# Kernel tuning notes

Measured on AMD Instinct MI355X. Metric: run time of the kernel, lower is better.

The kernel has to match this reference:

```python
import jax, jax.numpy as jnp
import numpy as np

B, T, L, D, H = 4, 1024, 1024, 1024, 16
HS = D // H          # head_size = 64
ROT = HS // 2        # rotary_ndims = 32


def setup_inputs() -> dict:
    key = jax.random.key(0)
    ks = jax.random.split(key, 8)
    x = jax.random.normal(ks[0], (B, T, D), dtype=jnp.float32)
    memory = jax.random.normal(ks[1], (B, L, D), dtype=jnp.float32)
    # RotaryEmbedding(rotary_ndims): inv_freq over ROT/2 freqs, emb = cat(freqs, freqs)
    inv_freq = 1.0 / (10000.0 ** (np.arange(0, ROT, 2, dtype=np.float32) / ROT))
    t = np.arange(T, dtype=np.float32)
    freqs = np.einsum('i,j->ij', t, inv_freq)            # [T, ROT/2]
    emb = np.concatenate([freqs, freqs], axis=-1)        # [T, ROT]
    RoPE = jnp.asarray(np.stack([np.cos(emb), np.sin(emb)]), dtype=jnp.float32)  # [2, T, ROT]
    s = 0.02
    Wq = jax.random.normal(ks[2], (D, D), dtype=jnp.float32) * s
    Wk = jax.random.normal(ks[3], (D, D), dtype=jnp.float32) * s
    Wv = jax.random.normal(ks[4], (D, D), dtype=jnp.float32) * s
    Wo = jax.random.normal(ks[5], (D, D), dtype=jnp.float32) * s
    bq = jnp.zeros((D,), jnp.float32)
    bk = jnp.zeros((D,), jnp.float32)
    bv = jnp.zeros((D,), jnp.float32)
    bo = jnp.zeros((D,), jnp.float32)
    return {"x": x, "memory": memory, "RoPE": RoPE,
            "Wq": Wq, "bq": bq, "Wk": Wk, "bk": bk,
            "Wv": Wv, "bv": bv, "Wo": Wo, "bo": bo}


def _rotate_half(u):
    u1, u2 = u[..., : u.shape[-1] // 2], u[..., u.shape[-1] // 2:]
    return jnp.concatenate([-u2, u1], axis=-1)


def _heads(y, n):  # [B, N, D] -> [B, H, N, HS]
    b = y.shape[0]
    return y.reshape(b, n, H, HS).transpose(0, 2, 1, 3)


def _attn(q, k, v):
    scale = 1.0 / jnp.sqrt(jnp.asarray(k.shape[-1], q.dtype))
    att = jnp.einsum('bhtd,bhsd->bhts', q, k) * scale
    att = jax.nn.softmax(att, axis=-1)
    return jnp.einsum('bhts,bhsd->bhtd', att, v)


def reference(x, memory, RoPE, Wq, bq, Wk, bk, Wv, bv, Wo, bo):
    b, t, d = x.shape
    l = memory.shape[1]
    cos, sin = RoPE[0][:t], RoPE[1][:t]  # [T, ROT], broadcasts over [B,H,T,ROT]

    # ---- self-attention with partial rotary ----
    q = _heads(x @ Wq.T + bq, t)
    k = _heads(x @ Wk.T + bk, t)
    v = _heads(x @ Wv.T + bv, t)
    q_rot, q_pass = q[..., :ROT], q[..., ROT:]
    k_rot, k_pass = k[..., :ROT], k[..., ROT:]
    q_rot = q_rot * cos + _rotate_half(q_rot) * sin
    k_rot = k_rot * cos + _rotate_half(k_rot) * sin
    q = jnp.concatenate([q_rot, q_pass], axis=-1)
    k = jnp.concatenate([k_rot, k_pass], axis=-1)
    y = _attn(q, k, v)                                   # [B,H,T,HS]
    y = y.transpose(0, 2, 1, 3).reshape(b, t, d)

    # ---- cross-attention (no rotary) ----
    q = _heads(y @ Wq.T + bq, t)
    k = _heads(memory @ Wk.T + bk, l)
    v = _heads(memory @ Wv.T + bv, l)
    y = _attn(q, k, v)
    y = y.transpose(0, 2, 1, 3).reshape(b, t, d)
    return y @ Wo.T + bo
```

## Files before the change

### kernel.cpp

```cpp
#include <hip/hip_runtime.h>

typedef unsigned short u16;
typedef __attribute__((ext_vector_type(8))) unsigned short ushort8;
typedef __attribute__((ext_vector_type(4))) unsigned short ushort4v;
typedef __attribute__((ext_vector_type(4))) float f32x4;
typedef __bf16 bf16x8 __attribute__((ext_vector_type(8)));


__device__ __forceinline__ u16 f2bf(float f) {
    unsigned u = __builtin_bit_cast(unsigned, f);
    unsigned r = u + 0x7fffu + ((u >> 16) & 1u);
    return (u16)(r >> 16);
}
__device__ __forceinline__ float bf2f(u16 h) {
    unsigned u = ((unsigned)h) << 16;
    return __builtin_bit_cast(float, u);
}

typedef const __attribute__((address_space(1))) unsigned gu32;
typedef __attribute__((address_space(3))) unsigned lu32;
__device__ __forceinline__ void gload16(const void* g, void* l) {
    __builtin_amdgcn_global_load_lds((gu32*)g, (lu32*)l, 16, 0, 0);
}

__global__ void k_f2b(const float4* __restrict__ in, u16* __restrict__ out, int n4) {
    int i = blockIdx.x * blockDim.x + threadIdx.x;
    if (i >= n4) return;
    float4 v = in[i];
    ushort4v r = { f2bf(v.x), f2bf(v.y), f2bf(v.z), f2bf(v.w) };
    *(ushort4v*)(out + (size_t)i * 4) = r;
}

template<int NSEG, int OUTBF>
__global__ __launch_bounds__(256) void k_gemm(const u16* __restrict__ Ap,
        const u16* __restrict__ w0, const u16* __restrict__ w1, const u16* __restrict__ w2,
        const float* __restrict__ b0, const float* __restrict__ b1, const float* __restrict__ b2,
        void* __restrict__ Cp, int colbase, int ldc) {
    __shared__ ushort8 sA[2][512];
    __shared__ ushort8 sB[2][512];
    const int tid = threadIdx.x, lane = tid & 63, w = tid >> 6;
    const int wr = w >> 1, wc = w & 1;

    const int nbx = gridDim.x;
    const int orig = blockIdx.y * nbx + blockIdx.x;
    const int qq = (nbx * gridDim.y) >> 3;
    const int logical = (orig & 7) * qq + (orig >> 3);
    const int bx = logical % nbx;
    const int m0 = (logical / nbx) * 128;

    const u16* W = w0; const float* bias = b0;
    if (NSEG >= 2 && bx >= 8)  { W = w1; bias = b1; }
    if (NSEG >= 3 && bx >= 16) { W = w2; bias = b2; }
    const int n0w = (bx & 7) * 128;
    const int outc0 = colbase + bx * 128;

    f32x4 acc[4][4] = {};

    const u16* asrc = Ap + (size_t)(m0 + 32 * w + (lane & 15)) * 1024 + (lane >> 4) * 8;
    const u16* bsrc = W  + (size_t)(n0w + 32 * w + (lane & 15)) * 1024 + (lane >> 4) * 8;

#define G_STAGE(p, kt) do { \
    gload16(asrc + (kt),             &sA[p][w * 128]); \
    gload16(asrc + (kt) + 16 * 1024, &sA[p][w * 128 + 64]); \
    gload16(bsrc + (kt),             &sB[p][w * 128]); \
    gload16(bsrc + (kt) + 16 * 1024, &sB[p][w * 128 + 64]); } while (0)

#define G_COMPUTE(p) do { \
    __builtin_amdgcn_s_barrier(); \
    asm volatile("" ::: "memory"); \
    bf16x8 af[4], bfr[4]; \
    for (int i = 0; i < 4; i++) af[i]  = __builtin_bit_cast(bf16x8, sA[p][(wr * 4 + i) * 64 + lane]); \
    for (int j = 0; j < 4; j++) bfr[j] = __builtin_bit_cast(bf16x8, sB[p][(wc * 4 + j) * 64 + lane]); \
    for (int i = 0; i < 4; i++) \
        for (int j = 0; j < 4; j++) \
            acc[i][j] = __builtin_amdgcn_mfma_f32_16x16x32_bf16(af[i], bfr[j], acc[i][j], 0, 0, 0); \
    asm volatile("" ::: "memory"); \
    __builtin_amdgcn_s_barrier(); } while (0)

    G_STAGE(0, 0);
    for (int t = 0; t < 30; t += 2) {
        G_STAGE(1, (t + 1) * 32);
        asm volatile("s_waitcnt vmcnt(4)" ::: "memory");
        G_COMPUTE(0);
        G_STAGE(0, (t + 2) * 32);
        asm volatile("s_waitcnt vmcnt(4)" ::: "memory");
        G_COMPUTE(1);
    }
    G_STAGE(1, 31 * 32);
    asm volatile("s_waitcnt vmcnt(4)" ::: "memory");
    G_COMPUTE(0);
    asm volatile("s_waitcnt vmcnt(0)" ::: "memory");
    G_COMPUTE(1);
#undef G_STAGE
#undef G_COMPUTE

    const int er = (lane >> 4) * 4, ec = lane & 15;
    for (int i = 0; i < 4; i++) {
        int grow_base = m0 + wr * 64 + i * 16 + er;
        for (int j = 0; j < 4; j++) {
            int cl = wc * 64 + j * 16 + ec;
            float bia = bias[n0w + cl];
            int gcol = outc0 + cl;
            for (int e = 0; e < 4; e++) {
                float v = acc[i][j][e] + bia;
                if (OUTBF) ((u16*)Cp)[(size_t)(grow_base + e) * ldc + gcol] = f2bf(v);
                else       ((float*)Cp)[(size_t)(grow_base + e) * ldc + gcol] = v;
            }
        }
    }
}

__global__ void k_rope(u16* __restrict__ QKV, const float* __restrict__ rope) {
    int idx = blockIdx.x * blockDim.x + threadIdx.x;
    int p = idx & 15;
    int h = (idx >> 4) & 15;
    int row = idx >> 8;
    int t = row & 1023;
    float c1 = rope[t * 32 + p];
    float c2 = rope[t * 32 + p + 16];
    const float* sinp = rope + 32768;
    float s1 = sinp[t * 32 + p];
    float s2 = sinp[t * 32 + p + 16];
    size_t base = (size_t)row * 3072 + h * 64;
    float u1 = bf2f(QKV[base + p]), u2 = bf2f(QKV[base + p + 16]);
    QKV[base + p]      = f2bf(u1 * c1 - u2 * s1);
    QKV[base + p + 16] = f2bf(u2 * c2 + u1 * s2);
    size_t kb = base + 1024;
    u1 = bf2f(QKV[kb + p]); u2 = bf2f(QKV[kb + p + 16]);
    QKV[kb + p]      = f2bf(u1 * c1 - u2 * s1);
    QKV[kb + p + 16] = f2bf(u2 * c2 + u1 * s2);
}

__global__ __launch_bounds__(256) void k_vt(const u16* __restrict__ Vb, u16* __restrict__ VTo) {
    __shared__ u16 tile[64][72];
    const int tid = threadIdx.x, lane = tid & 63, w = tid >> 6;
    const int sx = blockIdx.x, bh = blockIdx.y;
    const int b = bh >> 4, h = bh & 15;
    const u16* Vp = Vb + (size_t)(b * 1024 + sx * 64) * 3072 + h * 64;
    for (int it = 0; it < 2; it++) {
        int c = tid + it * 256, r = c >> 3, dc = c & 7;
        *(ushort8*)&tile[r][dc * 8] = *(const ushort8*)(Vp + (size_t)r * 3072 + dc * 8);
    }
    __syncthreads();
    u16* outp = VTo + (size_t)(bh * 64 + lane) * 1024 + sx * 64;
    for (int it = 0; it < 2; it++) {
        int sc = w + it * 4;
        ushort8 tv;
        for (int e = 0; e < 8; e++) tv[e] = tile[sc * 8 + e][lane];
        *(ushort8*)(outp + sc * 8) = tv;
    }
}

__global__ __launch_bounds__(256) void k_attn(const u16* __restrict__ Q, const u16* __restrict__ K,
                                              const u16* __restrict__ VTb, u16* __restrict__ O) {
    __shared__ ushort8 sK[2][512];
    __shared__ ushort8 sV[2][512];
    __shared__ ushort8 sP[512];

    const int tid = threadIdx.x, lane = tid & 63, w = tid >> 6;
    const int qt = blockIdx.x, h = blockIdx.y, b = blockIdx.z;
    const u16* Qh = Q + (size_t)(b * 1024 + qt * 64) * 3072 + h * 64;
    const u16* Kh = K + (size_t)(b * 1024) * 3072 + h * 64;
    const u16* VTh = VTb + (size_t)((b * 16 + h) * 64) * 1024;

    const u16* qa = Qh + (size_t)(16 * w + (lane & 15)) * 3072 + (lane >> 4) * 8;
    bf16x8 qf0 = __builtin_bit_cast(bf16x8, *(const ushort8*)qa);
    bf16x8 qf1 = __builtin_bit_cast(bf16x8, *(const ushort8*)(qa + 32));

    float m[4] = { -1e30f, -1e30f, -1e30f, -1e30f };
    float lsum[4] = { 0.f, 0.f, 0.f, 0.f };
    f32x4 o[4] = {};
    const float LS = 0.18033688011112042f;

    const int mrow = (lane >> 4) * 4;
    const int hi8 = (lane & 15) >> 3;
    const int se7 = lane & 7;

    const u16* ks = Kh + (size_t)(16 * w + (lane & 15)) * 3072 + (lane >> 4) * 8;
    const u16* vs = VTh + (size_t)(16 * w + (lane & 15)) * 1024 + (lane >> 4) * 8;

#define A_STAGE(p, s0) do { \
    gload16(ks + (size_t)(s0) * 3072,        &sK[p][w * 128]); \
    gload16(ks + (size_t)((s0) + 32) * 3072, &sK[p][w * 128 + 64]); \
    gload16(vs + (s0),                       &sV[p][w * 128]); \
    gload16(vs + (s0) + 32,                  &sV[p][w * 128 + 64]); } while (0)

#define A_COMPUTE(p) do { \
    __builtin_amdgcn_s_barrier(); \
    asm volatile("" ::: "memory"); \
    f32x4 sfr[4]; \
    for (int cb = 0; cb < 4; cb++) { \
        bf16x8 k0 = __builtin_bit_cast(bf16x8, sK[p][cb * 128 + lane]); \
        bf16x8 k1 = __builtin_bit_cast(bf16x8, sK[p][cb * 128 + 64 + lane]); \
        f32x4 a = {}; \
        a = __builtin_amdgcn_mfma_f32_16x16x32_bf16(qf0, k0, a, 0, 0, 0); \
        a = __builtin_amdgcn_mfma_f32_16x16x32_bf16(qf1, k1, a, 0, 0, 0); \
        sfr[cb] = a; \
    } \
    float rescale[4]; \
    for (int e = 0; e < 4; e++) { \
        float mx = fmaxf(fmaxf(sfr[0][e], sfr[1][e]), fmaxf(sfr[2][e], sfr[3][e])); \
        for (int off = 1; off < 16; off <<= 1) mx = fmaxf(mx, __shfl_xor(mx, off, 64)); \
        float mn = fmaxf(m[e], mx); \
        float r = __builtin_amdgcn_exp2f((m[e] - mn) * LS); \
        float rowsum = 0.f; \
        for (int cb = 0; cb < 4; cb++) { \
            float pv = __builtin_amdgcn_exp2f((sfr[cb][e] - mn) * LS); \
            sfr[cb][e] = pv; \
            rowsum += pv; \
        } \
        for (int off = 1; off < 16; off <<= 1) rowsum += __shfl_xor(rowsum, off, 64); \
        lsum[e] = lsum[e] * r + rowsum; \
        m[e] = mn; \
        rescale[e] = r; \
    } \
    for (int db = 0; db < 4; db++) \
        for (int e = 0; e < 4; e++) o[db][e] *= rescale[e]; \
    u16* sPw = ((u16*)sP) + w * 1024; \
    for (int cb = 0; cb < 4; cb++) { \
        int schunk = cb * 2 + hi8; \
        int cbase = (schunk >> 2) * 64 + (schunk & 3) * 16; \
        for (int e = 0; e < 4; e++) \
            sPw[(cbase + mrow + e) * 8 + se7] = f2bf(sfr[cb][e]); \
    } \
    bf16x8 pf0 = __builtin_bit_cast(bf16x8, sP[w * 128 + lane]); \
    bf16x8 pf1 = __builtin_bit_cast(bf16x8, sP[w * 128 + 64 + lane]); \
    for (int db = 0; db < 4; db++) { \
        bf16x8 v0 = __builtin_bit_cast(bf16x8, sV[p][db * 128 + lane]); \
        bf16x8 v1 = __builtin_bit_cast(bf16x8, sV[p][db * 128 + 64 + lane]); \
        o[db] = __builtin_amdgcn_mfma_f32_16x16x32_bf16(pf0, v0, o[db], 0, 0, 0); \
        o[db] = __builtin_amdgcn_mfma_f32_16x16x32_bf16(pf1, v1, o[db], 0, 0, 0); \
    } \
    asm volatile("" ::: "memory"); \
    __builtin_amdgcn_s_barrier(); } while (0)

    A_STAGE(0, 0);
    for (int t = 0; t < 14; t += 2) {
        A_STAGE(1, (t + 1) * 64);
        asm volatile("s_waitcnt vmcnt(4)" ::: "memory");
        A_COMPUTE(0);
        A_STAGE(0, (t + 2) * 64);
        asm volatile("s_waitcnt vmcnt(4)" ::: "memory");
        A_COMPUTE(1);
    }
    A_STAGE(1, 15 * 64);
    asm volatile("s_waitcnt vmcnt(4)" ::: "memory");
    A_COMPUTE(0);
    asm volatile("s_waitcnt vmcnt(0)" ::: "memory");
    A_COMPUTE(1);
#undef A_STAGE
#undef A_COMPUTE

    float rcp[4];
    for (int e = 0; e < 4; e++) rcp[e] = 1.0f / lsum[e];
    for (int db = 0; db < 4; db++) {
        int gcol = h * 64 + db * 16 + (lane & 15);
        for (int e = 0; e < 4; e++) {
            int grow = qt * 64 + 16 * w + mrow + e;
            O[(size_t)(b * 1024 + grow) * 1024 + gcol] = f2bf(o[db][e] * rcp[e]);
        }
    }
}

extern "C" void kernel_launch(void* const* d_in, const int* in_sizes, int n_in,
                              void* d_out, int out_size, void* d_ws, size_t ws_size,
                              hipStream_t stream) {
    const float* x    = (const float*)d_in[0];
    const float* mem  = (const float*)d_in[1];
    const float* rope = (const float*)d_in[2];
    const float* Wq   = (const float*)d_in[3];
    const float* bq   = (const float*)d_in[4];
    const float* Wk   = (const float*)d_in[5];
    const float* bk   = (const float*)d_in[6];
    const float* Wv   = (const float*)d_in[7];
    const float* bv   = (const float*)d_in[8];
    const float* Wo   = (const float*)d_in[9];
    const float* bo   = (const float*)d_in[10];
    float* out = (float*)d_out;

    char* ws = (char*)d_ws;
    const size_t MB = 1024 * 1024;
    u16* wqb = (u16*)(ws + 0 * MB);
    u16* wkb = (u16*)(ws + 2 * MB);
    u16* wvb = (u16*)(ws + 4 * MB);
    u16* wob = (u16*)(ws + 6 * MB);
    u16* QKV = (u16*)(ws + 8 * MB);
    u16* VT  = (u16*)(ws + 32 * MB);
    u16* SH  = (u16*)(ws + 40 * MB);

    k_f2b<<<1024, 256, 0, stream>>>((const float4*)Wq, wqb, 262144);
    k_f2b<<<1024, 256, 0, stream>>>((const float4*)Wk, wkb, 262144);
    k_f2b<<<1024, 256, 0, stream>>>((const float4*)Wv, wvb, 262144);
    k_f2b<<<1024, 256, 0, stream>>>((const float4*)Wo, wob, 262144);

    k_f2b<<<4096, 256, 0, stream>>>((const float4*)x, SH, 1048576);
    k_gemm<3, 1><<<dim3(24, 32), 256, 0, stream>>>(SH, wqb, wkb, wvb, bq, bk, bv,
                                                   QKV, 0, 3072);
    k_rope<<<4096, 256, 0, stream>>>(QKV, rope);
    k_vt<<<dim3(16, 64), 256, 0, stream>>>(QKV + 2048, VT);
    k_attn<<<dim3(16, 16, 4), 256, 0, stream>>>(QKV, QKV + 1024, VT, SH);

    k_gemm<1, 1><<<dim3(8, 32), 256, 0, stream>>>(SH, wqb, wqb, wqb, bq, bq, bq,
                                                  QKV, 0, 3072);
    k_f2b<<<4096, 256, 0, stream>>>((const float4*)mem, SH, 1048576);
    k_gemm<2, 1><<<dim3(16, 32), 256, 0, stream>>>(SH, wkb, wvb, wvb, bk, bv, bv,
                                                   QKV, 1024, 3072);
    k_vt<<<dim3(16, 64), 256, 0, stream>>>(QKV + 2048, VT);
    k_attn<<<dim3(16, 16, 4), 256, 0, stream>>>(QKV, QKV + 1024, VT, SH);

    k_gemm<1, 0><<<dim3(8, 32), 256, 0, stream>>>(SH, wob, wob, wob, bo, bo, bo,
                                                  out, 0, 1024);
}
```

Baseline: 409.0 us.

## Streamline attention softmax and pipeline barriers with DPP reductions and swizzled P

Replaces the paired s_barrier and manual vmcnt waits in the GEMM and attention loops with a single __syncthreads per stage. In attention, row max uses DPP row reductions instead of shuffles, and the row-sum reduction is deferred to the very end. The O rescale is skipped when no row max changed, and the P tile in LDS is XOR-swizzled to reduce bank conflicts. A block-index remap groups blocks by batch/head for better cache locality. The risk is that __syncthreads waits on all outstanding loads, which may reduce prefetch overlap.

```diff
diff --git a/kernel.cpp b/kernel.cpp
--- a/kernel.cpp
+++ b/kernel.cpp
@@ -21,6 +21,29 @@
 typedef __attribute__((address_space(3))) unsigned lu32;
 __device__ __forceinline__ void gload16(const void* g, void* l) {
     __builtin_amdgcn_global_load_lds((gu32*)g, (lu32*)l, 16, 0, 0);
+}
+
+__device__ __forceinline__ float dpp_max16(float x) {
+    int v = __builtin_bit_cast(int, x);
+    x = fmaxf(x, __builtin_bit_cast(float, __builtin_amdgcn_update_dpp(0, v, 0xB1, 0xF, 0xF, true)));
+    v = __builtin_bit_cast(int, x);
+    x = fmaxf(x, __builtin_bit_cast(float, __builtin_amdgcn_update_dpp(0, v, 0x4E, 0xF, 0xF, true)));
+    v = __builtin_bit_cast(int, x);
+    x = fmaxf(x, __builtin_bit_cast(float, __builtin_amdgcn_update_dpp(0, v, 0x141, 0xF, 0xF, true)));
+    v = __builtin_bit_cast(int, x);
+    x = fmaxf(x, __builtin_bit_cast(float, __builtin_amdgcn_update_dpp(0, v, 0x140, 0xF, 0xF, true)));
+    return x;
+}
+__device__ __forceinline__ float dpp_sum16(float x) {
+    int v = __builtin_bit_cast(int, x);
+    x += __builtin_bit_cast(float, __builtin_amdgcn_update_dpp(0, v, 0xB1, 0xF, 0xF, true));
+    v = __builtin_bit_cast(int, x);
+    x += __builtin_bit_cast(float, __builtin_amdgcn_update_dpp(0, v, 0x4E, 0xF, 0xF, true));
+    v = __builtin_bit_cast(int, x);
+    x += __builtin_bit_cast(float, __builtin_amdgcn_update_dpp(0, v, 0x141, 0xF, 0xF, true));
+    v = __builtin_bit_cast(int, x);
+    x += __builtin_bit_cast(float, __builtin_amdgcn_update_dpp(0, v, 0x140, 0xF, 0xF, true));
+    return x;
 }
 
 __global__ void k_f2b(const float4* __restrict__ in, u16* __restrict__ out, int n4) {
@@ -66,30 +89,26 @@
     gload16(bsrc + (kt) + 16 * 1024, &sB[p][w * 128 + 64]); } while (0)
 
 #define G_COMPUTE(p) do { \
-    __builtin_amdgcn_s_barrier(); \
-    asm volatile("" ::: "memory"); \
     bf16x8 af[4], bfr[4]; \
     for (int i = 0; i < 4; i++) af[i]  = __builtin_bit_cast(bf16x8, sA[p][(wr * 4 + i) * 64 + lane]); \
     for (int j = 0; j < 4; j++) bfr[j] = __builtin_bit_cast(bf16x8, sB[p][(wc * 4 + j) * 64 + lane]); \
     for (int i = 0; i < 4; i++) \
         for (int j = 0; j < 4; j++) \
-            acc[i][j] = __builtin_amdgcn_mfma_f32_16x16x32_bf16(af[i], bfr[j], acc[i][j], 0, 0, 0); \
-    asm volatile("" ::: "memory"); \
-    __builtin_amdgcn_s_barrier(); } while (0)
+            acc[i][j] = __builtin_amdgcn_mfma_f32_16x16x32_bf16(af[i], bfr[j], acc[i][j], 0, 0, 0); } while (0)
 
     G_STAGE(0, 0);
+    __syncthreads();
     for (int t = 0; t < 30; t += 2) {
         G_STAGE(1, (t + 1) * 32);
-        asm volatile("s_waitcnt vmcnt(4)" ::: "memory");
         G_COMPUTE(0);
+        __syncthreads();
         G_STAGE(0, (t + 2) * 32);
-        asm volatile("s_waitcnt vmcnt(4)" ::: "memory");
         G_COMPUTE(1);
+        __syncthreads();
     }
     G_STAGE(1, 31 * 32);
-    asm volatile("s_waitcnt vmcnt(4)" ::: "memory");
     G_COMPUTE(0);
-    asm volatile("s_waitcnt vmcnt(0)" ::: "memory");
+    __syncthreads();
     G_COMPUTE(1);
 #undef G_STAGE
 #undef G_COMPUTE
@@ -158,10 +177,15 @@
     __shared__ ushort8 sP[512];
 
     const int tid = threadIdx.x, lane = tid & 63, w = tid >> 6;
-    const int qt = blockIdx.x, h = blockIdx.y, b = blockIdx.z;
+    const int n = blockIdx.x + (blockIdx.y << 4) + (blockIdx.z << 8);
+    const int sl = n >> 3;
+    const int bh = ((n & 7) << 3) | (sl & 7);
+    const int qt = sl >> 3;
+    const int b = bh >> 4, h = bh & 15;
+
     const u16* Qh = Q + (size_t)(b * 1024 + qt * 64) * 3072 + h * 64;
     const u16* Kh = K + (size_t)(b * 1024) * 3072 + h * 64;
-    const u16* VTh = VTb + (size_t)((b * 16 + h) * 64) * 1024;
+    const u16* VTh = VTb + (size_t)(bh * 64) * 1024;
 
     const u16* qa = Qh + (size_t)(16 * w + (lane & 15)) * 3072 + (lane >> 4) * 8;
     bf16x8 qf0 = __builtin_bit_cast(bf16x8, *(const ushort8*)qa);
@@ -186,8 +210,6 @@
     gload16(vs + (s0) + 32,                  &sV[p][w * 128 + 64]); } while (0)
 
 #define A_COMPUTE(p) do { \
-    __builtin_amdgcn_s_barrier(); \
-    asm volatile("" ::: "memory"); \
     f32x4 sfr[4]; \
     for (int cb = 0; cb < 4; cb++) { \
         bf16x8 k0 = __builtin_bit_cast(bf16x8, sK[p][cb * 128 + lane]); \
@@ -197,62 +219,66 @@
         a = __builtin_amdgcn_mfma_f32_16x16x32_bf16(qf1, k1, a, 0, 0, 0); \
         sfr[cb] = a; \
     } \
-    float rescale[4]; \
+    float r4[4]; float need = 0.f; \
     for (int e = 0; e < 4; e++) { \
         float mx = fmaxf(fmaxf(sfr[0][e], sfr[1][e]), fmaxf(sfr[2][e], sfr[3][e])); \
-        for (int off = 1; off < 16; off <<= 1) mx = fmaxf(mx, __shfl_xor(mx, off, 64)); \
+        mx = dpp_max16(mx); \
         float mn = fmaxf(m[e], mx); \
-        float r = __builtin_amdgcn_exp2f((m[e] - mn) * LS); \
-        float rowsum = 0.f; \
+        need += mn - m[e]; \
+        r4[e] = __builtin_amdgcn_exp2f((m[e] - mn) * LS); \
+        float rs = 0.f; \
         for (int cb = 0; cb < 4; cb++) { \
             float pv = __builtin_amdgcn_exp2f((sfr[cb][e] - mn) * LS); \
             sfr[cb][e] = pv; \
-            rowsum += pv; \
+            rs += pv; \
         } \
-        for (int off = 1; off < 16; off <<= 1) rowsum += __shfl_xor(rowsum, off, 64); \
-        lsum[e] = lsum[e] * r + rowsum; \
+        lsum[e] = lsum[e] * r4[e] + rs; \
         m[e] = mn; \
-        rescale[e] = r; \
     } \
-    for (int db = 0; db < 4; db++) \
-        for (int e = 0; e < 4; e++) o[db][e] *= rescale[e]; \
+    if (__any(need > 0.f)) { \
+        for (int db = 0; db < 4; db++) \
+            for (int e = 0; e < 4; e++) o[db][e] *= r4[e]; \
+    } \
     u16* sPw = ((u16*)sP) + w * 1024; \
     for (int cb = 0; cb < 4; cb++) { \
         int schunk = cb * 2 + hi8; \
         int cbase = (schunk >> 2) * 64 + (schunk & 3) * 16; \
-        for (int e = 0; e < 4; e++) \
-            sPw[(cbase + mrow + e) * 8 + se7] = f2bf(sfr[cb][e]); \
+        for (int e = 0; e < 4; e++) { \
+            int ch = cbase + mrow + e; \
+            ch ^= (ch >> 3) & 7; \
+            sPw[ch * 8 + se7] = f2bf(sfr[cb][e]); \
+        } \
     } \
-    bf16x8 pf0 = __builtin_bit_cast(bf16x8, sP[w * 128 + lane]); \
-    bf16x8 pf1 = __builtin_bit_cast(bf16x8, sP[w * 128 + 64 + lane]); \
+    int c0 = lane ^ ((lane >> 3) & 7); \
+    int c1 = (64 + lane) ^ (((64 + lane) >> 3) & 7); \
+    bf16x8 pf0 = __builtin_bit_cast(bf16x8, sP[w * 128 + c0]); \
+    bf16x8 pf1 = __builtin_bit_cast(bf16x8, sP[w * 128 + c1]); \
     for (int db = 0; db < 4; db++) { \
         bf16x8 v0 = __builtin_bit_cast(bf16x8, sV[p][db * 128 + lane]); \
         bf16x8 v1 = __builtin_bit_cast(bf16x8, sV[p][db * 128 + 64 + lane]); \
         o[db] = __builtin_amdgcn_mfma_f32_16x16x32_bf16(pf0, v0, o[db], 0, 0, 0); \
         o[db] = __builtin_amdgcn_mfma_f32_16x16x32_bf16(pf1, v1, o[db], 0, 0, 0); \
-    } \
-    asm volatile("" ::: "memory"); \
-    __builtin_amdgcn_s_barrier(); } while (0)
+    } } while (0)
 
     A_STAGE(0, 0);
+    __syncthreads();
     for (int t = 0; t < 14; t += 2) {
         A_STAGE(1, (t + 1) * 64);
-        asm volatile("s_waitcnt vmcnt(4)" ::: "memory");
         A_COMPUTE(0);
+        __syncthreads();
         A_STAGE(0, (t + 2) * 64);
-        asm volatile("s_waitcnt vmcnt(4)" ::: "memory");
         A_COMPUTE(1);
+        __syncthreads();
     }
     A_STAGE(1, 15 * 64);
-    asm volatile("s_waitcnt vmcnt(4)" ::: "memory");
     A_COMPUTE(0);
-    asm volatile("s_waitcnt vmcnt(0)" ::: "memory");
+    __syncthreads();
     A_COMPUTE(1);
 #undef A_STAGE
 #undef A_COMPUTE
 
     float rcp[4];
-    for (int e = 0; e < 4; e++) rcp[e] = 1.0f / lsum[e];
+    for (int e = 0; e < 4; e++) rcp[e] = 1.0f / dpp_sum16(lsum[e]);
     for (int db = 0; db < 4; db++) {
         int gcol = h * 64 + db * 16 + (lane & 15);
         for (int e = 0; e < 4; e++) {
```

Result: faster. 377.4 us (-7.7%).
